# Kernel optimization log

Measured on AMD Instinct MI355X. Metric: run time of the kernel, lower is better.

## Reference

```python
import math
import jax, jax.numpy as jnp
import numpy as np

HIDDEN = 1024
N_HEADS = 16
HEAD = HIDDEN // N_HEADS
B = 2
L = 2048
STRIDE = 128
EXPR = 8
MAXPOS = 2048


def _checkpoint(wi):
    if wi % STRIDE == 0 and wi != 0:
        return wi - EXPR
    return (wi // STRIDE) * STRIDE + STRIDE - EXPR


def _subset_summaries(absolute_max):
    ci = _checkpoint(0)
    s = set()
    while ci <= absolute_max - 1:
        s |= set(range(ci, min(ci + EXPR + 1, absolute_max)))
        ci = _checkpoint(ci + STRIDE)
    return s


def build_sparse_mask(n, bidirectional=True):
    # Faithful numpy port of prepare_sparse_mask: -1e4 everywhere, 0 at allowed positions.
    mask = np.full((n, n), -10000.0, dtype=np.float32)
    global_summaries = _subset_summaries(n) if bidirectional else set()
    for i in range(n):
        absolute_max = n if bidirectional else i + 1
        rounded = ((i + STRIDE) // STRIDE) * STRIDE
        if i % STRIDE == 0 and i != 0:
            s1 = set(range(i - STRIDE, min(absolute_max, i + 1)))
        else:
            s1 = set(range(max(0, rounded - STRIDE), min(absolute_max, rounded + 1)))
        s2 = set() if bidirectional else _subset_summaries(absolute_max)
        idx = sorted(s1 | s2 | global_summaries)
        mask[i, idx] = 0.0
    return mask


def setup_inputs() -> dict:
    key = jax.random.key(0)
    ks = jax.random.split(key, 8)
    s = 1.0 / math.sqrt(HIDDEN)
    inp = {
        "hidden_states": jax.random.normal(ks[0], (B, L, HIDDEN), dtype=jnp.float32),
        "attention_mask": jnp.zeros((B, 1, 1, L), dtype=jnp.float32),
        "Wq": jax.random.normal(ks[1], (HIDDEN, HIDDEN), dtype=jnp.float32) * s,
        "bq": jnp.zeros((HIDDEN,), dtype=jnp.float32),
        "Wk": jax.random.normal(ks[2], (HIDDEN, HIDDEN), dtype=jnp.float32) * s,
        "bk": jnp.zeros((HIDDEN,), dtype=jnp.float32),
        "Wv": jax.random.normal(ks[3], (HIDDEN, HIDDEN), dtype=jnp.float32) * s,
        "bv": jnp.zeros((HIDDEN,), dtype=jnp.float32),
        "sparse_mask": jnp.asarray(build_sparse_mask(MAXPOS)[:L, :L]),
    }
    return inp


def _split_heads(x):  # [B, L, H] -> [B, nH, L, hd]
    b, l, _ = x.shape
    return x.reshape(b, l, N_HEADS, HEAD).transpose(0, 2, 1, 3)


def reference(hidden_states, attention_mask, Wq, bq, Wk, bk, Wv, bv, sparse_mask):
    q = _split_heads(hidden_states @ Wq + bq)
    k = _split_heads(hidden_states @ Wk + bk)
    v = _split_heads(hidden_states @ Wv + bv)
    scores = jnp.einsum("bhqd,bhkd->bhqk", q, k) / math.sqrt(HEAD)
    scores = scores + sparse_mask  # [L,L] broadcasts over [B,nH,L,L]
    scores = jnp.clip(scores, -10000.0, 10000.0)
    scores = scores + attention_mask
    probs = jax.nn.softmax(scores.astype(jnp.float32), axis=-1).astype(scores.dtype)
    # dropout prob = 0.0 -> identity
    ctx = jnp.einsum("bhqk,bhkd->bhqd", probs, v)
    return ctx.transpose(0, 2, 1, 3).reshape(hidden_states.shape[0], -1, HIDDEN)
```

## Files before the change

### kernel.cpp

```cpp
#include <hip/hip_runtime.h>

#define HID 1024
#define NH 16
#define HD 64
#define BB 2
#define LL 2048
#define GC 143
#define GP 192
#define AMT_PER_B 2240

typedef __attribute__((ext_vector_type(8))) __bf16 bf16x8;
typedef __attribute__((ext_vector_type(4))) float f32x4;
typedef __attribute__((ext_vector_type(4))) int i32x4;

__device__ __forceinline__ void gload_lds16(const void* g, void* l) {
  __builtin_amdgcn_global_load_lds((const __attribute__((address_space(1))) void*)g,
                                   (__attribute__((address_space(3))) void*)l, 16, 0, 0);
}

__device__ __forceinline__ unsigned int cvtpk(float lo, float hi) {
  unsigned int r;
  asm("v_cvt_pk_bf16_f32 %0, %1, %2" : "=v"(r) : "v"(lo), "v"(hi));
  return r;
}

__global__ __launch_bounds__(256) void prep_kernel(
    const float* __restrict__ hs, __bf16* __restrict__ hsb,
    const float* __restrict__ Wq, const float* __restrict__ Wk,
    const float* __restrict__ Wv, __bf16* __restrict__ wtb,
    const float* __restrict__ amask, unsigned int* __restrict__ zbase,
    float* __restrict__ amt) {
  int bx = blockIdx.x;
  int t = threadIdx.x;
  if (bx < 2048) {
    int i = bx * 256 + t;
    const float4* src = (const float4*)hs;
    float4 a = src[2 * i], b = src[2 * i + 1];
    bf16x8 v;
    v[0] = (__bf16)a.x; v[1] = (__bf16)a.y; v[2] = (__bf16)a.z; v[3] = (__bf16)a.w;
    v[4] = (__bf16)b.x; v[5] = (__bf16)b.y; v[6] = (__bf16)b.z; v[7] = (__bf16)b.w;
    ((bf16x8*)hsb)[i] = v;
  } else if (bx < 2048 + 768) {
    int z3 = bx - 2048;
    int kt = z3 & 15, nt = (z3 >> 4) & 15, z = z3 >> 8;
    const float* w = (z == 0) ? Wq : (z == 1) ? Wk : Wv;
    __bf16* dst = wtb + (size_t)z * HID * HID;
    __shared__ __bf16 tile[64][66];
    int cr = t & 63, rr = t >> 6;
#pragma unroll
    for (int it = 0; it < 16; it++) {
      int r = it * 4 + rr;
      tile[cr][r] = (__bf16)w[(size_t)(kt * 64 + r) * HID + nt * 64 + cr];
    }
    __syncthreads();
#pragma unroll
    for (int it = 0; it < 16; it++) {
      int r = it * 4 + rr;
      dst[(size_t)(nt * 64 + r) * HID + kt * 64 + cr] = tile[r][cr];
    }
  } else if (bx < 2048 + 768 + 1536) {
    int i = (bx - 2816) * 256 + t;
    zbase[i] = 0u;
  } else {
    int idx = (bx - 4352) * 256 + t;
    if (idx < BB * AMT_PER_B) {
      int b = idx / AMT_PER_B, r = idx % AMT_PER_B;
      float val;
      if (r < GP) {
        int k = r / 9, j = r - 9 * k;
        val = (r < GC) ? (amask[b * LL + 120 + 128 * k + j] - 20.f) : -1e5f;
      } else {
        int r2 = r - GP;
        int w = r2 >> 7, off = r2 & 127;
        bool gcol = (off >= 120) || (off == 0 && w != 0);
        val = gcol ? -1e5f : (amask[b * LL + w * 128 + off] - 20.f);
      }
      amt[idx] = val;
    }
  }
}

__global__ __launch_bounds__(256, 2) void qkv_gemm_kernel(
    const __bf16* __restrict__ hsb, const __bf16* __restrict__ wtb,
    const float* __restrict__ bq, const float* __restrict__ bk,
    const float* __restrict__ bv, __bf16* __restrict__ qb,
    __bf16* __restrict__ kkb, __bf16* __restrict__ vtb,
    __bf16* __restrict__ kgb, __bf16* __restrict__ vgb) {
  int nt = blockIdx.x, mt = blockIdx.y, which = blockIdx.z;
  const __bf16* wt = wtb + (size_t)which * HID * HID;
  const float* bias = (which == 0) ? bq : (which == 1) ? bk : bv;

  __shared__ __bf16 a_lds[128 * 64];
  __shared__ __bf16 b_lds[128 * 64];

  int tid = threadIdx.x;
  int wave = tid >> 6, lane = tid & 63;
  int wm = wave >> 1, wn = wave & 1;
  int lrow = lane & 15, lgr = lane >> 4, g = lane & 7;

  f32x4 acc[4][4];
#pragma unroll
  for (int i = 0; i < 4; i++)
#pragma unroll
    for (int j = 0; j < 4; j++) acc[i][j] = f32x4{0.f, 0.f, 0.f, 0.f};

  for (int kk = 0; kk < HID; kk += 64) {
#pragma unroll
    for (int i = 0; i < 4; i++) {
      int r = (wave * 4 + i) * 8 + (lane >> 3);
      int gs = (g ^ (r & 7)) * 8;
      gload_lds16(hsb + (size_t)(mt * 128 + r) * HID + kk + gs,
                  &a_lds[(wave * 4 + i) * 512]);
      gload_lds16(wt + (size_t)(nt * 128 + r) * HID + kk + gs,
                  &b_lds[(wave * 4 + i) * 512]);
    }
    __syncthreads();
#pragma unroll
    for (int kf = 0; kf < 2; kf++) {
      bf16x8 af[4], bfr[4];
#pragma unroll
      for (int mr = 0; mr < 4; mr++) {
        int row = wm * 64 + mr * 16 + lrow;
        af[mr] = *(const bf16x8*)((const char*)a_lds + row * 128 +
                                  ((kf * 64 + lgr * 16) ^ ((row & 7) << 4)));
      }
#pragma unroll
      for (int nr = 0; nr < 4; nr++) {
        int row = wn * 64 + nr * 16 + lrow;
        bfr[nr] = *(const bf16x8*)((const char*)b_lds + row * 128 +
                                   ((kf * 64 + lgr * 16) ^ ((row & 7) << 4)));
      }
#pragma unroll
      for (int mr = 0; mr < 4; mr++)
#pragma unroll
        for (int nr = 0; nr < 4; nr++)
          acc[mr][nr] = __builtin_amdgcn_mfma_f32_16x16x32_bf16(
              af[mr], bfr[nr], acc[mr][nr], 0, 0, 0);
    }
    __syncthreads();
  }

#pragma unroll
  for (int nr = 0; nr < 4; nr++) {
    int n = nt * 128 + wn * 64 + nr * 16 + lrow;
    float bsv = bias[n];
    int hh = n >> 6, d = n & 63;
#pragma unroll
    for (int mr = 0; mr < 4; mr++) {
#pragma unroll
      for (int reg = 0; reg < 4; reg++) {
        int m = mt * 128 + wm * 64 + mr * 16 + lgr * 4 + reg;
        int bidx = m >> 11, l = m & 2047;
        float val = acc[mr][nr][reg] + bsv;
        int c7 = l & 127;
        bool isg = (c7 >= 120) || (c7 == 0 && l != 0);
        int cidx = (c7 >= 120) ? ((l >> 7) * 9 + (c7 - 120)) : (((l >> 7) - 1) * 9 + 8);
        if (which == 0) {
          val *= 0.125f;
          qb[((size_t)(bidx * NH + hh) * LL + l) * HD + d] = (__bf16)val;
        } else if (which == 1) {
          __bf16 bv16 = (__bf16)val;
          kkb[((size_t)(bidx * NH + hh) * LL + l) * HD + d] = bv16;
          if (isg) kgb[((size_t)(bidx * NH + hh) * GP + cidx) * HD + d] = bv16;
        } else {
          __bf16 bv16 = (__bf16)val;
          vtb[((size_t)(bidx * NH + hh) * HD + d) * LL + l] = bv16;
          if (isg) vgb[((size_t)(bidx * NH + hh) * HD + d) * GP + cidx] = bv16;
        }
      }
    }
  }
}

__global__ __launch_bounds__(256, 4) void attn_kernel(
    const __bf16* __restrict__ qb, const __bf16* __restrict__ kkb,
    const __bf16* __restrict__ vtb, const __bf16* __restrict__ kgb,
    const __bf16* __restrict__ vgb, const float* __restrict__ amt,
    float* __restrict__ out) {
  __shared__ __bf16 kbuf[2][64 * 64];
  __shared__ __bf16 vbuf[2][64 * 64];

  int qt = blockIdx.x, hh = blockIdx.y, b = blockIdx.z;
  int tid = threadIdx.x, wave = tid >> 6, lane = tid & 63;
  int lrow = lane & 15, lgr = lane >> 4, g = lane & 7;

  const __bf16* qbh = qb + (size_t)(b * NH + hh) * LL * HD;
  const __bf16* kbh = kkb + (size_t)(b * NH + hh) * LL * HD;
  const __bf16* vth = vtb + (size_t)(b * NH + hh) * HD * LL;
  const __bf16* kgh = kgb + (size_t)(b * NH + hh) * GP * HD;
  const __bf16* vgh = vgb + (size_t)(b * NH + hh) * HD * GP;

  int shift = (qt == 32) ? 0 : 1;
  int qt2 = (qt == 32) ? 0 : qt;
  int W = (qt2 >> 1) * 128;
  const float* amt_b = amt + b * AMT_PER_B;
  const float* amt_l = amt_b + GP + (qt2 >> 1) * 128;

  int qrow = qt2 * 64 + shift + wave * 16 + lrow;
  int qld = (qrow > LL - 1) ? (LL - 1) : qrow;
  bf16x8 qf0 = *(const bf16x8*)(qbh + (size_t)qld * HD + lgr * 8);
  bf16x8 qf1 = *(const bf16x8*)(qbh + (size_t)qld * HD + 32 + lgr * 8);

  int va = ((lgr & 1) * 32 + lrow) * 4;
  int vb = va + 64;
  bool lohalf = (lane < 32);

  float l_part = 0.f;
  f32x4 o_acc[4];
#pragma unroll
  for (int i = 0; i < 4; i++) o_acc[i] = f32x4{0.f, 0.f, 0.f, 0.f};

#define STAGE(IT, BI)                                                     \
  do {                                                                    \
    const __bf16 *ks_, *vs_;                                              \
    int vst_;                                                             \
    if ((IT) < 3) {                                                       \
      ks_ = kgh + (size_t)((IT)*64) * HD;                                 \
      vs_ = vgh + (IT)*64;                                                \
      vst_ = GP;                                                          \
    } else {                                                              \
      int cb_ = W + ((IT)-3) * 64;                                        \
      ks_ = kbh + (size_t)cb_ * HD;                                       \
      vs_ = vth + cb_;                                                    \
      vst_ = LL;                                                          \
    }                                                                     \
    _Pragma("unroll")                                                     \
    for (int i_ = 0; i_ < 2; i_++) {                                      \
      int r_ = (wave * 2 + i_) * 8 + (lane >> 3);                         \
      int gs_ = (g ^ (r_ & 7)) * 8;                                       \
      gload_lds16(ks_ + (size_t)r_ * HD + gs_, &kbuf[BI][(wave * 2 + i_) * 512]); \
      gload_lds16(vs_ + (size_t)r_ * vst_ + gs_, &vbuf[BI][(wave * 2 + i_) * 512]); \
    }                                                                     \
  } while (0)

  STAGE(0, 0);
  __syncthreads();

#pragma unroll
  for (int it = 0; it < 5; it++) {
    int cur = it & 1;
    if (it < 4) STAGE(it + 1, cur ^ 1);

    const __bf16* k_lds = kbuf[cur];
    const __bf16* v_lds = vbuf[cur];

    const float* abase = (it < 3) ? (amt_b + it * 64) : (amt_l + (it - 3) * 64);
    f32x4 ad[4];
#pragma unroll
    for (int nr = 0; nr < 4; nr++)
      ad[nr] = *(const f32x4*)(abase + nr * 16 + lgr * 4);

    f32x4 s[4];
#pragma unroll
    for (int nr = 0; nr < 4; nr++) {
      int row = nr * 16 + lrow;
      bf16x8 kf0 = *(const bf16x8*)((const char*)k_lds + row * 128 +
                                    ((lgr * 16) ^ ((row & 7) << 4)));
      bf16x8 kf1 = *(const bf16x8*)((const char*)k_lds + row * 128 +
                                    ((64 + lgr * 16) ^ ((row & 7) << 4)));
      f32x4 z = f32x4{0.f, 0.f, 0.f, 0.f};
      z = __builtin_amdgcn_mfma_f32_16x16x32_bf16(kf0, qf0, z, 0, 0, 0);
      z = __builtin_amdgcn_mfma_f32_16x16x32_bf16(kf1, qf1, z, 0, 0, 0);
      s[nr] = z;
    }

#pragma unroll
    for (int nr = 0; nr < 4; nr++) {
#pragma unroll
      for (int reg = 0; reg < 4; reg++) {
        float v = fminf(fmaxf(s[nr][reg], -10000.f), 10000.f) + ad[nr][reg];
        float p = __expf(v);
        s[nr][reg] = p;
        l_part += p;
      }
    }

    unsigned int c00 = cvtpk(s[0][0], s[0][1]), c01 = cvtpk(s[0][2], s[0][3]);
    unsigned int c10 = cvtpk(s[1][0], s[1][1]), c11 = cvtpk(s[1][2], s[1][3]);
    unsigned int c20 = cvtpk(s[2][0], s[2][1]), c21 = cvtpk(s[2][2], s[2][3]);
    unsigned int c30 = cvtpk(s[3][0], s[3][1]), c31 = cvtpk(s[3][2], s[3][3]);

    i32x4 w0, w1;
    {
      int a0 = __builtin_amdgcn_ds_bpermute(va, (int)c00);
      int a1 = __builtin_amdgcn_ds_bpermute(va, (int)c10);
      w0[0] = lohalf ? a0 : a1;
      int b0 = __builtin_amdgcn_ds_bpermute(va, (int)c01);
      int b1 = __builtin_amdgcn_ds_bpermute(va, (int)c11);
      w0[1] = lohalf ? b0 : b1;
      int d0 = __builtin_amdgcn_ds_bpermute(vb, (int)c00);
      int d1 = __builtin_amdgcn_ds_bpermute(vb, (int)c10);
      w0[2] = lohalf ? d0 : d1;
      int e0 = __builtin_amdgcn_ds_bpermute(vb, (int)c01);
      int e1 = __builtin_amdgcn_ds_bpermute(vb, (int)c11);
      w0[3] = lohalf ? e0 : e1;

      int f0 = __builtin_amdgcn_ds_bpermute(va, (int)c20);
      int f1 = __builtin_amdgcn_ds_bpermute(va, (int)c30);
      w1[0] = lohalf ? f0 : f1;
      int g0 = __builtin_amdgcn_ds_bpermute(va, (int)c21);
      int g1 = __builtin_amdgcn_ds_bpermute(va, (int)c31);
      w1[1] = lohalf ? g0 : g1;
      int h0 = __builtin_amdgcn_ds_bpermute(vb, (int)c20);
      int h1 = __builtin_amdgcn_ds_bpermute(vb, (int)c30);
      w1[2] = lohalf ? h0 : h1;
      int i0 = __builtin_amdgcn_ds_bpermute(vb, (int)c21);
      int i1 = __builtin_amdgcn_ds_bpermute(vb, (int)c31);
      w1[3] = lohalf ? i0 : i1;
    }
    bf16x8 pb0 = __builtin_bit_cast(bf16x8, w0);
    bf16x8 pb1 = __builtin_bit_cast(bf16x8, w1);

#pragma unroll
    for (int nd = 0; nd < 4; nd++) {
      int row = nd * 16 + lrow;
      bf16x8 vf0 = *(const bf16x8*)((const char*)v_lds + row * 128 +
                                    ((lgr * 16) ^ ((row & 7) << 4)));
      bf16x8 vf1 = *(const bf16x8*)((const char*)v_lds + row * 128 +
                                    ((64 + lgr * 16) ^ ((row & 7) << 4)));
      o_acc[nd] = __builtin_amdgcn_mfma_f32_16x16x32_bf16(vf0, pb0, o_acc[nd], 0, 0, 0);
      o_acc[nd] = __builtin_amdgcn_mfma_f32_16x16x32_bf16(vf1, pb1, o_acc[nd], 0, 0, 0);
    }
    __syncthreads();
  }
#undef STAGE

  l_part += __shfl_xor(l_part, 16);
  l_part += __shfl_xor(l_part, 32);
  float rl = 1.f / l_part;

  if (qrow < LL) {
    float* obase = out + ((size_t)b * LL + qrow) * HID + hh * HD + lgr * 4;
#pragma unroll
    for (int nd = 0; nd < 4; nd++) {
      float4 ov;
      ov.x = o_acc[nd][0] * rl;
      ov.y = o_acc[nd][1] * rl;
      ov.z = o_acc[nd][2] * rl;
      ov.w = o_acc[nd][3] * rl;
      *(float4*)(obase + nd * 16) = ov;
    }
  }
}

extern "C" void kernel_launch(void* const* d_in, const int* in_sizes, int n_in,
                              void* d_out, int out_size, void* d_ws, size_t ws_size,
                              hipStream_t stream) {
  (void)in_sizes; (void)n_in; (void)out_size; (void)ws_size;
  const float* hs = (const float*)d_in[0];
  const float* amask = (const float*)d_in[1];
  const float* Wq = (const float*)d_in[2];
  const float* bq = (const float*)d_in[3];
  const float* Wk = (const float*)d_in[4];
  const float* bk = (const float*)d_in[5];
  const float* Wv = (const float*)d_in[6];
  const float* bv = (const float*)d_in[7];
  float* out = (float*)d_out;

  char* ws = (char*)d_ws;
  __bf16* hsb = (__bf16*)(ws);
  __bf16* wtb = (__bf16*)(ws + 8388608);
  __bf16* qb  = (__bf16*)(ws + 14680064);
  __bf16* kb  = (__bf16*)(ws + 23068672);
  __bf16* vtb = (__bf16*)(ws + 31457280);
  __bf16* kgb = (__bf16*)(ws + 39845888);
  __bf16* vgb = (__bf16*)(ws + 40632320);
  float*  amt = (float*)(ws + 41418752);

  hipLaunchKernelGGL(prep_kernel, dim3(4370), dim3(256), 0, stream,
                     hs, hsb, Wq, Wk, Wv, wtb, amask, (unsigned int*)kgb, amt);
  hipLaunchKernelGGL(qkv_gemm_kernel, dim3(8, 32, 3), dim3(256), 0, stream,
                     hsb, wtb, bq, bk, bv, qb, kb, vtb, kgb, vgb);
  hipLaunchKernelGGL(attn_kernel, dim3(33, NH, BB), dim3(256), 0, stream,
                     qb, kb, vtb, kgb, vgb, amt, out);
}
```

Before: 70.59 us.

## Process two 16-row query tiles per wave to reuse staged K/V tiles

Each attention block now covers 128 query rows instead of 64, with every wave handling two 16-row query sub-tiles that share the same K/V fragments read from LDS. The grid is halved from 33 to 17 blocks along the query axis, which halves the number of K/V tile loads from global memory and LDS per query. The final barrier after the last iteration is also dropped. In exchange each wave needs more registers and fewer blocks are launched (17x16x2), which may leave the GPU under-occupied.

```diff
diff --git a/kernel.cpp b/kernel.cpp
--- a/kernel.cpp
+++ b/kernel.cpp
@@ -190,25 +190,32 @@
   const __bf16* kgh = kgb + (size_t)(b * NH + hh) * GP * HD;
   const __bf16* vgh = vgb + (size_t)(b * NH + hh) * HD * GP;
 
-  int shift = (qt == 32) ? 0 : 1;
-  int qt2 = (qt == 32) ? 0 : qt;
-  int W = (qt2 >> 1) * 128;
+  int shift = (qt == 16) ? 0 : 1;
+  int qt2 = (qt == 16) ? 0 : qt;
+  int W = qt2 * 128;
   const float* amt_b = amt + b * AMT_PER_B;
-  const float* amt_l = amt_b + GP + (qt2 >> 1) * 128;
-
-  int qrow = qt2 * 64 + shift + wave * 16 + lrow;
-  int qld = (qrow > LL - 1) ? (LL - 1) : qrow;
-  bf16x8 qf0 = *(const bf16x8*)(qbh + (size_t)qld * HD + lgr * 8);
-  bf16x8 qf1 = *(const bf16x8*)(qbh + (size_t)qld * HD + 32 + lgr * 8);
+  const float* amt_l = amt_b + GP + qt2 * 128;
+
+  int qrowA = qt2 * 128 + shift + wave * 32 + lrow;
+  int qrowB = qrowA + 16;
+  int qldA = (qrowA > LL - 1) ? (LL - 1) : qrowA;
+  int qldB = (qrowB > LL - 1) ? (LL - 1) : qrowB;
+  bf16x8 qA0 = *(const bf16x8*)(qbh + (size_t)qldA * HD + lgr * 8);
+  bf16x8 qA1 = *(const bf16x8*)(qbh + (size_t)qldA * HD + 32 + lgr * 8);
+  bf16x8 qB0 = *(const bf16x8*)(qbh + (size_t)qldB * HD + lgr * 8);
+  bf16x8 qB1 = *(const bf16x8*)(qbh + (size_t)qldB * HD + 32 + lgr * 8);
 
   int va = ((lgr & 1) * 32 + lrow) * 4;
   int vb = va + 64;
   bool lohalf = (lane < 32);
 
-  float l_part = 0.f;
-  f32x4 o_acc[4];
-#pragma unroll
-  for (int i = 0; i < 4; i++) o_acc[i] = f32x4{0.f, 0.f, 0.f, 0.f};
+  float lA = 0.f, lB = 0.f;
+  f32x4 oA[4], oB[4];
+#pragma unroll
+  for (int i = 0; i < 4; i++) {
+    oA[i] = f32x4{0.f, 0.f, 0.f, 0.f};
+    oB[i] = f32x4{0.f, 0.f, 0.f, 0.f};
+  }
 
 #define STAGE(IT, BI)                                                     \
   do {                                                                    \
@@ -250,7 +257,7 @@
     for (int nr = 0; nr < 4; nr++)
       ad[nr] = *(const f32x4*)(abase + nr * 16 + lgr * 4);
 
-    f32x4 s[4];
+    f32x4 sA[4], sB[4];
 #pragma unroll
     for (int nr = 0; nr < 4; nr++) {
       int row = nr * 16 + lrow;
@@ -258,30 +265,38 @@
                                     ((lgr * 16) ^ ((row & 7) << 4)));
       bf16x8 kf1 = *(const bf16x8*)((const char*)k_lds + row * 128 +
                                     ((64 + lgr * 16) ^ ((row & 7) << 4)));
-      f32x4 z = f32x4{0.f, 0.f, 0.f, 0.f};
-      z = __builtin_amdgcn_mfma_f32_16x16x32_bf16(kf0, qf0, z, 0, 0, 0);
-      z = __builtin_amdgcn_mfma_f32_16x16x32_bf16(kf1, qf1, z, 0, 0, 0);
-      s[nr] = z;
+      f32x4 zA = f32x4{0.f, 0.f, 0.f, 0.f};
+      zA = __builtin_amdgcn_mfma_f32_16x16x32_bf16(kf0, qA0, zA, 0, 0, 0);
+      zA = __builtin_amdgcn_mfma_f32_16x16x32_bf16(kf1, qA1, zA, 0, 0, 0);
+      sA[nr] = zA;
+      f32x4 zB = f32x4{0.f, 0.f, 0.f, 0.f};
+      zB = __builtin_amdgcn_mfma_f32_16x16x32_bf16(kf0, qB0, zB, 0, 0, 0);
+      zB = __builtin_amdgcn_mfma_f32_16x16x32_bf16(kf1, qB1, zB, 0, 0, 0);
+      sB[nr] = zB;
     }
 
 #pragma unroll
     for (int nr = 0; nr < 4; nr++) {
 #pragma unroll
       for (int reg = 0; reg < 4; reg++) {
-        float v = fminf(fmaxf(s[nr][reg], -10000.f), 10000.f) + ad[nr][reg];
-        float p = __expf(v);
-        s[nr][reg] = p;
-        l_part += p;
+        float vA = fminf(fmaxf(sA[nr][reg], -10000.f), 10000.f) + ad[nr][reg];
+        float pA = __expf(vA);
+        sA[nr][reg] = pA;
+        lA += pA;
+        float vB = fminf(fmaxf(sB[nr][reg], -10000.f), 10000.f) + ad[nr][reg];
+        float pB = __expf(vB);
+        sB[nr][reg] = pB;
+        lB += pB;
       }
     }
 
-    unsigned int c00 = cvtpk(s[0][0], s[0][1]), c01 = cvtpk(s[0][2], s[0][3]);
-    unsigned int c10 = cvtpk(s[1][0], s[1][1]), c11 = cvtpk(s[1][2], s[1][3]);
-    unsigned int c20 = cvtpk(s[2][0], s[2][1]), c21 = cvtpk(s[2][2], s[2][3]);
-    unsigned int c30 = cvtpk(s[3][0], s[3][1]), c31 = cvtpk(s[3][2], s[3][3]);
-
-    i32x4 w0, w1;
+    bf16x8 pbA0, pbA1, pbB0, pbB1;
     {
+      unsigned int c00 = cvtpk(sA[0][0], sA[0][1]), c01 = cvtpk(sA[0][2], sA[0][3]);
+      unsigned int c10 = cvtpk(sA[1][0], sA[1][1]), c11 = cvtpk(sA[1][2], sA[1][3]);
+      unsigned int c20 = cvtpk(sA[2][0], sA[2][1]), c21 = cvtpk(sA[2][2], sA[2][3]);
+      unsigned int c30 = cvtpk(sA[3][0], sA[3][1]), c31 = cvtpk(sA[3][2], sA[3][3]);
+      i32x4 w0, w1;
       int a0 = __builtin_amdgcn_ds_bpermute(va, (int)c00);
       int a1 = __builtin_amdgcn_ds_bpermute(va, (int)c10);
       w0[0] = lohalf ? a0 : a1;
@@ -294,7 +309,6 @@
       int e0 = __builtin_amdgcn_ds_bpermute(vb, (int)c01);
       int e1 = __builtin_amdgcn_ds_bpermute(vb, (int)c11);
       w0[3] = lohalf ? e0 : e1;
-
       int f0 = __builtin_amdgcn_ds_bpermute(va, (int)c20);
       int f1 = __builtin_amdgcn_ds_bpermute(va, (int)c30);
       w1[0] = lohalf ? f0 : f1;
@@ -307,9 +321,42 @@
       int i0 = __builtin_amdgcn_ds_bpermute(vb, (int)c21);
       int i1 = __builtin_amdgcn_ds_bpermute(vb, (int)c31);
       w1[3] = lohalf ? i0 : i1;
-    }
-    bf16x8 pb0 = __builtin_bit_cast(bf16x8, w0);
-    bf16x8 pb1 = __builtin_bit_cast(bf16x8, w1);
+      pbA0 = __builtin_bit_cast(bf16x8, w0);
+      pbA1 = __builtin_bit_cast(bf16x8, w1);
+    }
+    {
+      unsigned int c00 = cvtpk(sB[0][0], sB[0][1]), c01 = cvtpk(sB[0][2], sB[0][3]);
+      unsigned int c10 = cvtpk(sB[1][0], sB[1][1]), c11 = cvtpk(sB[1][2], sB[1][3]);
+      unsigned int c20 = cvtpk(sB[2][0], sB[2][1]), c21 = cvtpk(sB[2][2], sB[2][3]);
+      unsigned int c30 = cvtpk(sB[3][0], sB[3][1]), c31 = cvtpk(sB[3][2], sB[3][3]);
+      i32x4 w0, w1;
+      int a0 = __builtin_amdgcn_ds_bpermute(va, (int)c00);
+      int a1 = __builtin_amdgcn_ds_bpermute(va, (int)c10);
+      w0[0] = lohalf ? a0 : a1;
+      int b0 = __builtin_amdgcn_ds_bpermute(va, (int)c01);
+      int b1 = __builtin_amdgcn_ds_bpermute(va, (int)c11);
+      w0[1] = lohalf ? b0 : b1;
+      int d0 = __builtin_amdgcn_ds_bpermute(vb, (int)c00);
+      int d1 = __builtin_amdgcn_ds_bpermute(vb, (int)c10);
+      w0[2] = lohalf ? d0 : d1;
+      int e0 = __builtin_amdgcn_ds_bpermute(vb, (int)c01);
+      int e1 = __builtin_amdgcn_ds_bpermute(vb, (int)c11);
+      w0[3] = lohalf ? e0 : e1;
+      int f0 = __builtin_amdgcn_ds_bpermute(va, (int)c20);
+      int f1 = __builtin_amdgcn_ds_bpermute(va, (int)c30);
+      w1[0] = lohalf ? f0 : f1;
+      int g0 = __builtin_amdgcn_ds_bpermute(va, (int)c21);
+      int g1 = __builtin_amdgcn_ds_bpermute(va, (int)c31);
+      w1[1] = lohalf ? g0 : g1;
+      int h0 = __builtin_amdgcn_ds_bpermute(vb, (int)c20);
+      int h1 = __builtin_amdgcn_ds_bpermute(vb, (int)c30);
+      w1[2] = lohalf ? h0 : h1;
+      int i0 = __builtin_amdgcn_ds_bpermute(vb, (int)c21);
+      int i1 = __builtin_amdgcn_ds_bpermute(vb, (int)c31);
+      w1[3] = lohalf ? i0 : i1;
+      pbB0 = __builtin_bit_cast(bf16x8, w0);
+      pbB1 = __builtin_bit_cast(bf16x8, w1);
+    }
 
 #pragma unroll
     for (int nd = 0; nd < 4; nd++) {
@@ -318,26 +365,42 @@
                                     ((lgr * 16) ^ ((row & 7) << 4)));
       bf16x8 vf1 = *(const bf16x8*)((const char*)v_lds + row * 128 +
                                     ((64 + lgr * 16) ^ ((row & 7) << 4)));
-      o_acc[nd] = __builtin_amdgcn_mfma_f32_16x16x32_bf16(vf0, pb0, o_acc[nd], 0, 0, 0);
-      o_acc[nd] = __builtin_amdgcn_mfma_f32_16x16x32_bf16(vf1, pb1, o_acc[nd], 0, 0, 0);
-    }
-    __syncthreads();
+      oA[nd] = __builtin_amdgcn_mfma_f32_16x16x32_bf16(vf0, pbA0, oA[nd], 0, 0, 0);
+      oA[nd] = __builtin_amdgcn_mfma_f32_16x16x32_bf16(vf1, pbA1, oA[nd], 0, 0, 0);
+      oB[nd] = __builtin_amdgcn_mfma_f32_16x16x32_bf16(vf0, pbB0, oB[nd], 0, 0, 0);
+      oB[nd] = __builtin_amdgcn_mfma_f32_16x16x32_bf16(vf1, pbB1, oB[nd], 0, 0, 0);
+    }
+    if (it < 4) __syncthreads();
   }
 #undef STAGE
 
-  l_part += __shfl_xor(l_part, 16);
-  l_part += __shfl_xor(l_part, 32);
-  float rl = 1.f / l_part;
-
-  if (qrow < LL) {
-    float* obase = out + ((size_t)b * LL + qrow) * HID + hh * HD + lgr * 4;
+  lA += __shfl_xor(lA, 16);
+  lA += __shfl_xor(lA, 32);
+  lB += __shfl_xor(lB, 16);
+  lB += __shfl_xor(lB, 32);
+  float rlA = 1.f / lA, rlB = 1.f / lB;
+
+  if (qrowA < LL) {
+    float* obase = out + ((size_t)b * LL + qrowA) * HID + hh * HD + lgr * 4;
 #pragma unroll
     for (int nd = 0; nd < 4; nd++) {
       float4 ov;
-      ov.x = o_acc[nd][0] * rl;
-      ov.y = o_acc[nd][1] * rl;
-      ov.z = o_acc[nd][2] * rl;
-      ov.w = o_acc[nd][3] * rl;
+      ov.x = oA[nd][0] * rlA;
+      ov.y = oA[nd][1] * rlA;
+      ov.z = oA[nd][2] * rlA;
+      ov.w = oA[nd][3] * rlA;
+      *(float4*)(obase + nd * 16) = ov;
+    }
+  }
+  if (qrowB < LL) {
+    float* obase = out + ((size_t)b * LL + qrowB) * HID + hh * HD + lgr * 4;
+#pragma unroll
+    for (int nd = 0; nd < 4; nd++) {
+      float4 ov;
+      ov.x = oB[nd][0] * rlB;
+      ov.y = oB[nd][1] * rlB;
+      ov.z = oB[nd][2] * rlB;
+      ov.w = oB[nd][3] * rlB;
       *(float4*)(obase + nd * 16) = ov;
     }
   }
@@ -371,6 +434,6 @@
                      hs, hsb, Wq, Wk, Wv, wtb, amask, (unsigned int*)kgb, amt);
   hipLaunchKernelGGL(qkv_gemm_kernel, dim3(8, 32, 3), dim3(256), 0, stream,
                      hsb, wtb, bq, bk, bv, qb, kb, vtb, kgb, vgb);
-  hipLaunchKernelGGL(attn_kernel, dim3(33, NH, BB), dim3(256), 0, stream,
+  hipLaunchKernelGGL(attn_kernel, dim3(17, NH, BB), dim3(256), 0, stream,
                      qb, kb, vtb, kgb, vgb, amt, out);
 }
```

After: 70.27 us. Within noise of the previous version (-0.4%).
